# Kernel tuning notes

Measured on AMD Instinct MI355X. Metric: run time of the kernel, lower is better.

## Reference

```python
import jax, jax.numpy as jnp
import numpy as np

SOFT_CAP = 20.0
NEG_BIG = -1e9


def setup_inputs() -> dict:
    key = jax.random.key(0)
    kq, kk, kv = jax.random.split(key, 3)
    T, H, D = 3072, 16, 128
    lens = np.array([1024, 768, 640, 640], dtype=np.int32)  # sums to T, max 1024
    cu = np.concatenate([[0], np.cumsum(lens)]).astype(np.int32)
    q = jax.random.normal(kq, (T, H, D), dtype=jnp.float32)
    k = jax.random.normal(kk, (T, H, D), dtype=jnp.float32)
    v = jax.random.normal(kv, (T, H, D), dtype=jnp.float32)
    return {
        "q": q, "k": k, "v": v,
        "cu_seqlens_q": jnp.asarray(cu), "cu_seqlens_k": jnp.asarray(cu),
        "max_seqlen_q": 1024, "max_seqlen_k": 1024,
    }


def _varlen_attention(q, k, v, cu_q, cu_k, S_q, S_k):
    # q,k,v: [T, H, D] packed; cu_*: [B+1] prefix sums; S_*: static max seqlens
    T, H, D = q.shape
    B = cu_q.shape[0] - 1
    lens_q = cu_q[1:] - cu_q[:-1]  # [B]
    lens_k = cu_k[1:] - cu_k[:-1]
    ar_q = jnp.arange(S_q)
    ar_k = jnp.arange(S_k)
    # pad packed tokens into [B, S, H, D]
    idx_q = jnp.clip(cu_q[:-1, None] + ar_q[None, :], 0, T - 1)  # [B, S_q]
    idx_k = jnp.clip(cu_k[:-1, None] + ar_k[None, :], 0, k.shape[0] - 1)
    mask_k = ar_k[None, :] < lens_k[:, None]  # [B, S_k] valid keys
    qp = q[idx_q]  # [B, S_q, H, D]
    kp = k[idx_k]  # [B, S_k, H, D]
    vp = v[idx_k]
    scale = 1.0 / jnp.sqrt(jnp.float32(D))
    scores = jnp.einsum("bqhd,bkhd->bhqk", qp, kp) * scale  # [B, H, S_q, S_k] fp32
    scores = jnp.tanh(scores / SOFT_CAP) * SOFT_CAP  # logit soft-cap
    scores = jnp.where(mask_k[:, None, None, :], scores, NEG_BIG)
    w = jax.nn.softmax(scores, axis=-1)
    out = jnp.einsum("bhqk,bkhd->bqhd", w, vp)  # [B, S_q, H, D]
    # unpad back to packed [T, H, D]
    t = jnp.arange(T)
    seg = jnp.searchsorted(cu_q, t, side="right") - 1  # sequence id per token
    pos = seg * S_q + (t - cu_q[seg])
    return out.reshape(B * S_q, H, D)[pos]


def reference(q, k, v, cu_seqlens_q, cu_seqlens_k, max_seqlen_q, max_seqlen_k):
    return _varlen_attention(q, k, v, cu_seqlens_q, cu_seqlens_k,
                             int(max_seqlen_q), int(max_seqlen_k))
```

## Files before the change

kernel.cpp:

```cpp
#include <hip/hip_runtime.h>

#define H_ 16
#define D_ 128

typedef __attribute__((ext_vector_type(4))) float f32x4;
typedef __attribute__((ext_vector_type(8))) short bf8_t;
typedef __attribute__((ext_vector_type(4))) unsigned int u32x4;

__device__ __forceinline__ unsigned cvt_pk(float a, float b) {
  unsigned r;
  asm("v_cvt_pk_bf16_f32 %0, %1, %2" : "=v"(r) : "v"(a), "v"(b));
  return r;
}

__device__ __forceinline__ float exp2a(float x) {
  float r;
  asm("v_exp_f32 %0, %1" : "=v"(r) : "v"(x));
  return r;
}

__device__ __forceinline__ bf8_t cvt8(const f32x4 a, const f32x4 b) {
  u32x4 r;
  r[0] = cvt_pk(a[0], a[1]); r[1] = cvt_pk(a[2], a[3]);
  r[2] = cvt_pk(b[0], b[1]); r[3] = cvt_pk(b[2], b[3]);
  return __builtin_bit_cast(bf8_t, r);
}

__global__ __launch_bounds__(128)
void conv_kv(const float* __restrict__ K, const float* __restrict__ V,
             const int* __restrict__ cuk, short* __restrict__ Kbf,
             short* __restrict__ Vt, int B, int T) {
  const int J0 = blockIdx.x * 8;
  const int h  = blockIdx.y;
  int b = 0;
  while (b + 1 < B && J0 >= cuk[b + 1]) ++b;
  const int k0 = cuk[b];

  {
    const int g = J0 + (threadIdx.x >> 4);
    const int c = threadIdx.x & 15;
    const int sub = c ^ ((g - k0) & 7);
    const float* src = K + ((size_t)g * H_ + h) * D_ + sub * 8;
    *(bf8_t*)(Kbf + ((size_t)g * H_ + h) * D_ + c * 8) =
        cvt8(*(const f32x4*)src, *(const f32x4*)(src + 4));
  }
  {
    const int d  = threadIdx.x;
    const int j0 = J0 - k0;
    const int base = k0 + (j0 >> 6) * 64 + 32 * ((j0 >> 5) & 1) + 4 * ((j0 >> 3) & 3);
    float v[8];
    #pragma unroll
    for (int s = 0; s < 8; ++s)
      v[s] = V[((size_t)(base + 16 * (s >> 2) + (s & 3)) * H_ + h) * D_ + d];
    u32x4 w;
    w[0] = cvt_pk(v[0], v[1]); w[1] = cvt_pk(v[2], v[3]);
    w[2] = cvt_pk(v[4], v[5]); w[3] = cvt_pk(v[6], v[7]);
    *(u32x4*)(Vt + ((size_t)h * D_ + d) * T + J0) = w;
  }
}

__global__ __launch_bounds__(256, 2)
void fa_main(const float* __restrict__ Q, const short* __restrict__ Kbf,
             const short* __restrict__ Vt, const int* __restrict__ cuq,
             const int* __restrict__ cuk, float* __restrict__ O, int B, int T) {
  __shared__ __align__(16) short k_lds[2][64 * 128];
  __shared__ __align__(16) short v_lds[2][64 * 128];

  const int slot = blockIdx.x;
  int bmax = 0, nmax = 0, tot = 0;
  for (int bb = 0; bb < B; ++bb) {
    const int nk = (cuk[bb + 1] - cuk[bb] + 63) >> 6;
    if (nk > nmax) { nmax = nk; bmax = bb; }
    tot += ((cuq[bb + 1] - cuq[bb] + 127) >> 7) * 16;
  }
  if (slot >= tot) return;
  const int L = ((cuq[bmax + 1] - cuq[bmax] + 127) >> 7) * 16;
  const int halfS = (tot - L) >> 1;

  int b = -1, item = 0;
  if (slot >= halfS && slot < halfS + L) {
    b = bmax; item = slot - halfS;
  } else {
    int sidx = (slot < halfS) ? slot : slot - L;
    for (int bb = 0; bb < B; ++bb) {
      if (bb == bmax) continue;
      const int it = ((cuq[bb + 1] - cuq[bb] + 127) >> 7) * 16;
      if (sidx < it) { b = bb; item = sidx; break; }
      sidx -= it;
    }
    if (b < 0) return;
  }
  const int qt = item >> 4;
  const int h  = item & 15;

  const int q0   = cuq[b];
  const int lenq = cuq[b + 1] - q0;
  const int k0   = cuk[b];
  const int lenk = cuk[b + 1] - k0;
  const int nkt  = (lenk + 63) >> 6;

  const int tid  = threadIdx.x;
  const int wave = tid >> 6;
  const int lane = tid & 63;
  const int lo   = lane & 15;
  const int gp   = lane >> 4;

  const int qrow_base = qt * 128 + wave * 32;

  bf8_t qf[2][4];
  #pragma unroll
  for (int s2 = 0; s2 < 2; ++s2) {
    const int qr = qrow_base + s2 * 16 + lo;
    const int qg = q0 + (qr < lenq ? qr : lenq - 1);
    const float* qp = Q + ((size_t)qg * H_ + h) * D_;
    #pragma unroll
    for (int db = 0; db < 4; ++db) {
      const f32x4 a = *reinterpret_cast<const f32x4*>(qp + db * 32 + gp * 8);
      const f32x4 c = *reinterpret_cast<const f32x4*>(qp + db * 32 + gp * 8 + 4);
      qf[s2][db] = cvt8(a, c);
    }
  }

  f32x4 acc[2][8];
  #pragma unroll
  for (int s2 = 0; s2 < 2; ++s2)
    #pragma unroll
    for (int i = 0; i < 8; ++i) acc[s2][i] = f32x4{0.f, 0.f, 0.f, 0.f};
  float lpa[2] = {0.f, 0.f}, lpb[2] = {0.f, 0.f};

  const int skey = tid >> 4;
  const int ssub = tid & 15;
  const int vd5  = tid >> 3;
  const int vcp  = tid & 7;
  const int vclog = vcp ^ (vd5 & 7);
  const short* KbH = Kbf + h * D_ + ssub * 8;
  const short* VtH = Vt + ((size_t)h * D_) * T;

  const float cz = 0.0044194174f;
  const float ce = 28.853901f;

  u32x4 krb[4], vrb[4];
  auto issue_loads = [&](int kb) {
    #pragma unroll
    for (int i = 0; i < 4; ++i) {
      const int kk = kb + skey + 16 * i;
      const size_t gk = (size_t)(k0 + (kk < lenk ? kk : lenk - 1));
      krb[i] = *(const u32x4*)(KbH + gk * (H_ * D_));
    }
    #pragma unroll
    for (int i = 0; i < 4; ++i) {
      const int d = i * 32 + vd5;
      vrb[i] = *(const u32x4*)(VtH + (size_t)d * T + (k0 + kb + vclog * 8));
    }
  };
  auto write_tile = [&](int buf) {
    char* kb2 = (char*)k_lds[buf];
    char* vb2 = (char*)v_lds[buf];
    #pragma unroll
    for (int i = 0; i < 4; ++i)
      *(u32x4*)(kb2 + (skey + 16 * i) * 256 + ssub * 16) = krb[i];
    #pragma unroll
    for (int i = 0; i < 4; ++i)
      *(u32x4*)(vb2 + (i * 32 + vd5) * 128 + vcp * 16) = vrb[i];
  };

  issue_loads(0);
  write_tile(0);
  __syncthreads();

  for (int kt = 0; kt < nkt; ++kt) {
    const int kb = kt * 64;
    char* kbase = (char*)k_lds[kt & 1];
    char* vtb   = (char*)v_lds[kt & 1];

    if (kt + 1 < nkt) issue_loads(kb + 64);
    __builtin_amdgcn_sched_barrier(0);

    f32x4 s[2][4];
    #pragma unroll
    for (int s2 = 0; s2 < 2; ++s2)
      #pragma unroll
      for (int kq = 0; kq < 4; ++kq) s[s2][kq] = f32x4{0.f, 0.f, 0.f, 0.f};
    __builtin_amdgcn_s_setprio(1);
    #pragma unroll
    for (int db = 0; db < 4; ++db) {
      #pragma unroll
      for (int kq = 0; kq < 4; ++kq) {
        const bf8_t kf = *(const bf8_t*)(kbase + (kq * 16 + lo) * 256 +
                                         (((4 * db + gp) ^ (lo & 7)) << 4));
        s[0][kq] = __builtin_amdgcn_mfma_f32_16x16x32_bf16(kf, qf[0][db], s[0][kq], 0, 0, 0);
        s[1][kq] = __builtin_amdgcn_mfma_f32_16x16x32_bf16(kf, qf[1][db], s[1][kq], 0, 0, 0);
      }
    }
    __builtin_amdgcn_s_setprio(0);

    #pragma unroll
    for (int s2 = 0; s2 < 2; ++s2) {
      #pragma unroll
      for (int kq = 0; kq < 4; ++kq) {
        const int keyb = kb + 16 * kq + 4 * gp;
        #pragma unroll
        for (int r = 0; r < 4; ++r) {
          float z = s[s2][kq][r] * cz;
          z = __builtin_amdgcn_fmed3f(z, -0.68f, 0.68f);
          const float z2 = z * z;
          const float pol = fmaf(z2, fmaf(z2, 0.13333334f, -0.33333334f), 1.0f);
          float p = exp2a(fmaf(z * ce, pol, -ce));
          p = (keyb + r < lenk) ? p : 0.0f;
          if (kq & 1) lpb[s2] += p; else lpa[s2] += p;
          s[s2][kq][r] = p;
        }
      }
    }

    u32x4 pf[2][2];
    #pragma unroll
    for (int s2 = 0; s2 < 2; ++s2) {
      #pragma unroll
      for (int ks = 0; ks < 2; ++ks) {
        pf[s2][ks][0] = cvt_pk(s[s2][2 * ks][0], s[s2][2 * ks][1]);
        pf[s2][ks][1] = cvt_pk(s[s2][2 * ks][2], s[s2][2 * ks][3]);
        pf[s2][ks][2] = cvt_pk(s[s2][2 * ks + 1][0], s[s2][2 * ks + 1][1]);
        pf[s2][ks][3] = cvt_pk(s[s2][2 * ks + 1][2], s[s2][2 * ks + 1][3]);
      }
    }

    __builtin_amdgcn_s_setprio(1);
    #pragma unroll
    for (int ks = 0; ks < 2; ++ks) {
      #pragma unroll
      for (int nt = 0; nt < 8; ++nt) {
        const int d = nt * 16 + lo;
        const bf8_t vf = *(const bf8_t*)(
            vtb + d * 128 + ((((ks << 2) + gp) ^ (lo & 7)) << 4));
        acc[0][nt] = __builtin_amdgcn_mfma_f32_16x16x32_bf16(
            __builtin_bit_cast(bf8_t, pf[0][ks]), vf, acc[0][nt], 0, 0, 0);
        acc[1][nt] = __builtin_amdgcn_mfma_f32_16x16x32_bf16(
            __builtin_bit_cast(bf8_t, pf[1][ks]), vf, acc[1][nt], 0, 0, 0);
      }
    }
    __builtin_amdgcn_s_setprio(0);

    if (kt + 1 < nkt) write_tile((kt + 1) & 1);
    __syncthreads();
  }

  #pragma unroll
  for (int s2 = 0; s2 < 2; ++s2) {
    float lp = lpa[s2] + lpb[s2];
    lp += __shfl_xor(lp, 16);
    lp += __shfl_xor(lp, 32);
    const float inv_full = 1.0f / lp;
    #pragma unroll
    for (int r = 0; r < 4; ++r) {
      const float inv_l = __shfl(inv_full, 4 * gp + r);
      const int qr = qrow_base + s2 * 16 + 4 * gp + r;
      if (qr < lenq) {
        float* op = O + ((size_t)(q0 + qr) * H_ + h) * D_;
        #pragma unroll
        for (int nt = 0; nt < 8; ++nt)
          op[nt * 16 + lo] = acc[s2][nt][r] * inv_l;
      }
    }
  }
}

extern "C" void kernel_launch(void* const* d_in, const int* in_sizes, int n_in,
                              void* d_out, int out_size, void* d_ws, size_t ws_size,
                              hipStream_t stream) {
  const float* Q  = (const float*)d_in[0];
  const float* K  = (const float*)d_in[1];
  const float* V  = (const float*)d_in[2];
  const int* cuq  = (const int*)d_in[3];
  const int* cuk  = (const int*)d_in[4];
  float* out      = (float*)d_out;
  const int B = in_sizes[3] - 1;
  const int T = in_sizes[0] / (H_ * D_);

  short* Kbf = (short*)d_ws;
  short* Vt  = Kbf + (size_t)T * H_ * D_;

  conv_kv<<<dim3(T / 8, H_), 128, 0, stream>>>(K, V, cuk, Kbf, Vt, B, T);
  const int maxItems = 16 * (T / 128 + B);
  fa_main<<<maxItems, 256, 0, stream>>>(Q, Kbf, Vt, cuq, cuk, out, B, T);
}
```

Baseline: 64.48 us.

## Compute softmax row sums via MFMA, fold soft-cap constants, split masked tiles

Row sums of the softmax weights are now accumulated with an extra MFMA against a vector of bf16 ones, which replaces the per-element scalar adds and the final cross-lane shuffles. The tanh polynomial constants are folded into the score scale so each element needs fewer multiplies. Full tiles skip the key-length mask test. The next tile's LDS write is moved before the PV MFMAs so it can overlap them. The ones-MFMA sums bf16-rounded probabilities, which slightly changes normalization precision, and it adds MFMA work.

```diff
diff --git a/kernel.cpp b/kernel.cpp
--- a/kernel.cpp
+++ b/kernel.cpp
@@ -126,7 +126,11 @@
   for (int s2 = 0; s2 < 2; ++s2)
     #pragma unroll
     for (int i = 0; i < 8; ++i) acc[s2][i] = f32x4{0.f, 0.f, 0.f, 0.f};
-  float lpa[2] = {0.f, 0.f}, lpb[2] = {0.f, 0.f};
+  f32x4 acc_l[2] = {f32x4{0.f, 0.f, 0.f, 0.f}, f32x4{0.f, 0.f, 0.f, 0.f}};
+
+  bf8_t onesf;
+  #pragma unroll
+  for (int i = 0; i < 8; ++i) onesf[i] = (short)0x3F80;
 
   const int skey = tid >> 4;
   const int ssub = tid & 15;
@@ -136,8 +140,11 @@
   const short* KbH = Kbf + h * D_ + ssub * 8;
   const short* VtH = Vt + ((size_t)h * D_) * T;
 
-  const float cz = 0.0044194174f;
-  const float ce = 28.853901f;
+  const float cy  = 0.12752749f;
+  const float ce  = 28.853901f;
+  const float ycl = 19.620652f;
+  const float c3p = -4.0037686e-4f;
+  const float c4p = 1.9236228e-7f;
 
   u32x4 krb[4], vrb[4];
   auto issue_loads = [&](int kb) {
@@ -194,21 +201,37 @@
     }
     __builtin_amdgcn_s_setprio(0);
 
-    #pragma unroll
-    for (int s2 = 0; s2 < 2; ++s2) {
-      #pragma unroll
-      for (int kq = 0; kq < 4; ++kq) {
-        const int keyb = kb + 16 * kq + 4 * gp;
+    const bool fullTile = (kb + 64 <= lenk);
+    if (fullTile) {
+      #pragma unroll
+      for (int s2 = 0; s2 < 2; ++s2) {
         #pragma unroll
-        for (int r = 0; r < 4; ++r) {
-          float z = s[s2][kq][r] * cz;
-          z = __builtin_amdgcn_fmed3f(z, -0.68f, 0.68f);
-          const float z2 = z * z;
-          const float pol = fmaf(z2, fmaf(z2, 0.13333334f, -0.33333334f), 1.0f);
-          float p = exp2a(fmaf(z * ce, pol, -ce));
-          p = (keyb + r < lenk) ? p : 0.0f;
-          if (kq & 1) lpb[s2] += p; else lpa[s2] += p;
-          s[s2][kq][r] = p;
+        for (int kq = 0; kq < 4; ++kq) {
+          #pragma unroll
+          for (int r = 0; r < 4; ++r) {
+            float y = s[s2][kq][r] * cy;
+            y = __builtin_amdgcn_fmed3f(y, -ycl, ycl);
+            const float u = y * y;
+            const float pol = fmaf(u, fmaf(u, c4p, c3p), 1.0f);
+            s[s2][kq][r] = exp2a(fmaf(y, pol, -ce));
+          }
+        }
+      }
+    } else {
+      #pragma unroll
+      for (int s2 = 0; s2 < 2; ++s2) {
+        #pragma unroll
+        for (int kq = 0; kq < 4; ++kq) {
+          const int keyb = kb + 16 * kq + 4 * gp;
+          #pragma unroll
+          for (int r = 0; r < 4; ++r) {
+            float y = s[s2][kq][r] * cy;
+            y = __builtin_amdgcn_fmed3f(y, -ycl, ycl);
+            const float u = y * y;
+            const float pol = fmaf(u, fmaf(u, c4p, c3p), 1.0f);
+            float p = exp2a(fmaf(y, pol, -ce));
+            s[s2][kq][r] = (keyb + r < lenk) ? p : 0.0f;
+          }
         }
       }
     }
@@ -225,9 +248,15 @@
       }
     }
 
+    if (kt + 1 < nkt) write_tile((kt + 1) & 1);
+
     __builtin_amdgcn_s_setprio(1);
     #pragma unroll
     for (int ks = 0; ks < 2; ++ks) {
+      acc_l[0] = __builtin_amdgcn_mfma_f32_16x16x32_bf16(
+          __builtin_bit_cast(bf8_t, pf[0][ks]), onesf, acc_l[0], 0, 0, 0);
+      acc_l[1] = __builtin_amdgcn_mfma_f32_16x16x32_bf16(
+          __builtin_bit_cast(bf8_t, pf[1][ks]), onesf, acc_l[1], 0, 0, 0);
       #pragma unroll
       for (int nt = 0; nt < 8; ++nt) {
         const int d = nt * 16 + lo;
@@ -241,19 +270,14 @@
     }
     __builtin_amdgcn_s_setprio(0);
 
-    if (kt + 1 < nkt) write_tile((kt + 1) & 1);
     __syncthreads();
   }
 
   #pragma unroll
   for (int s2 = 0; s2 < 2; ++s2) {
-    float lp = lpa[s2] + lpb[s2];
-    lp += __shfl_xor(lp, 16);
-    lp += __shfl_xor(lp, 32);
-    const float inv_full = 1.0f / lp;
     #pragma unroll
     for (int r = 0; r < 4; ++r) {
-      const float inv_l = __shfl(inv_full, 4 * gp + r);
+      const float inv_l = 1.0f / acc_l[s2][r];
       const int qr = qrow_base + s2 * 16 + 4 * gp + r;
       if (qr < lenq) {
         float* op = O + ((size_t)(q0 + qr) * H_ + h) * D_;
```

Result: faster. 61.54 us (median of 2 runs) (-4.6%).
